# Kernel optimization log

Measured on AMD Instinct MI355X. Metric: run time of the kernel, lower is better.

Reference implementation:

```python
import jax, jax.numpy as jnp
import numpy as np


def setup_inputs() -> dict:
    key = jax.random.key(0)
    ks = jax.random.split(key, 9)
    B, C, H, W = 4, 256, 128, 128
    d = C // 8
    x = jax.random.normal(ks[0], (B, C, H, W), jnp.float32)
    wq = jax.random.normal(ks[1], (d, C), jnp.float32) * 0.05
    bq = jax.random.normal(ks[2], (d,), jnp.float32) * 0.05
    wk = jax.random.normal(ks[3], (d, C), jnp.float32) * 0.05
    bk = jax.random.normal(ks[4], (d,), jnp.float32) * 0.05
    wv = jax.random.normal(ks[5], (d, C), jnp.float32) * 0.05
    bv = jax.random.normal(ks[6], (d,), jnp.float32) * 0.05
    wp = jax.random.normal(ks[7], (C, d, 3, 3), jnp.float32) * 0.05
    gamma = jax.random.normal(ks[8], (1,), jnp.float32)
    return dict(x=x, wq=wq, bq=bq, wk=wk, bk=bk, wv=wv, bv=bv, wp=wp, gamma=gamma)


def reference(x, wq, bq, wk, bk, wv, bv, wp, gamma):
    B, C, H, W = x.shape
    d = wq.shape[0]  # C // 8
    N = H * W
    # 1x1 convs expressed as channel matmuls
    q = jnp.einsum('bchw,dc->bdhw', x, wq) + bq[None, :, None, None]
    k = jnp.einsum('bchw,dc->bdhw', x, wk) + bk[None, :, None, None]
    v = jnp.einsum('bchw,dc->bdhw', x, wv) + bv[None, :, None, None]
    Q = q.reshape(B, d, N)
    K = k.reshape(B, d, N)
    V = v.reshape(B, d, N)
    # channel-channel energy: [B, d, d]
    energy = jnp.einsum('bdn,ben->bde', Q, K)
    energy_new = jnp.max(energy, axis=-1, keepdims=True) - energy
    attention = jax.nn.softmax(energy_new, axis=-1)
    out = jnp.einsum('bde,ben->bdn', attention, V).reshape(B, d, H, W)
    # 3x3 conv (no bias) + exact GELU
    out = jax.lax.conv_general_dilated(
        out, wp, window_strides=(1, 1), padding='SAME',
        dimension_numbers=('NCHW', 'OIHW', 'NCHW'))
    out = jax.nn.gelu(out, approximate=False)
    return gamma[0] * out + x
```

## Files before the change

### kernel.cpp

```cpp
#include <hip/hip_runtime.h>
#include <hip/hip_bf16.h>
#include <math.h>

#define BB 4
#define CC 256
#define HH 128
#define WW 128
#define NN (HH*WW)
#define DD 32

#define AOT_CI   44
#define AOT_ROWE (130*AOT_CI)
#define AOT_IMGE (130*AOT_ROWE)
#define AOT_BYTES ((size_t)BB*AOT_IMGE*2)
#define AOT_ALLOC (AOT_BYTES + 1024)

#define WT_BYTES (9*256*AOT_CI*2)

#define PATCH_SZ 45760
#define WSLAB    22528
#define CONV_LDS (PATCH_SZ + 2*WSLAB)
#define EPI_PITCH 260

#define ASWZ_BYTES 98304
#define AHALF      49152
#define QK2        132

typedef __attribute__((ext_vector_type(8)))  short bf16x8;
typedef __attribute__((ext_vector_type(4)))  float f32x4;
typedef __attribute__((ext_vector_type(16))) float f32x16;

__device__ inline void async_copy16(void* lds, const void* g) {
    __builtin_amdgcn_global_load_lds(
        (const __attribute__((address_space(1))) unsigned int*)g,
        (__attribute__((address_space(3))) unsigned int*)lds, 16, 0, 0);
}

__device__ inline unsigned short f2bf(float f) {
    __hip_bfloat16 h = __float2bfloat16(f);
    return *reinterpret_cast<unsigned short*>(&h);
}

__device__ inline void split2(float v, unsigned short& h, unsigned short& l) {
    __hip_bfloat16 hb = __float2bfloat16(v);
    float r = v - __bfloat162float(hb);
    __hip_bfloat16 lb = __float2bfloat16(r);
    h = *reinterpret_cast<unsigned short*>(&hb);
    l = *reinterpret_cast<unsigned short*>(&lb);
}

__device__ inline bf16x8 ld_frag8(const char* p) {
    union { bf16x8 v; short4 h[2]; } u;
    u.h[0] = *(const short4*)(p);
    u.h[1] = *(const short4*)(p + 8);
    return u.v;
}

__device__ inline float gelu_fast(float v) {
    float a = fabsf(v) * 0.70710678118654752f;
    float t = __fdividef(1.0f, fmaf(0.3275911f, a, 1.0f));
    float p = t * fmaf(t, fmaf(t, fmaf(t, fmaf(t, 1.061405429f, -1.453152027f),
                                       1.421413741f), -0.284496736f), 0.254829592f);
    float e = 1.0f - p * __expf(-a * a);
    float erfv = (v < 0.0f) ? -e : e;
    return 0.5f * v * (1.0f + erfv);
}

__global__ __launch_bounds__(256) void prep_kernel(
    const float* __restrict__ wp, unsigned short* __restrict__ Wt,
    const float* __restrict__ wq, const float* __restrict__ wk,
    const float* __restrict__ wv, unsigned short* __restrict__ Aswz,
    unsigned short* __restrict__ AOT)
{
    const int blk = blockIdx.x;
    if (blk < 288) {
        int i = blk*256 + threadIdx.x;
        int kk = i / (256*32);
        int r  = i % (256*32);
        int co = r >> 5, ci = r & 31;
        float v = wp[((size_t)co*32 + ci)*9 + kk];
        Wt[((size_t)kk*256 + co)*AOT_CI + ci] = f2bf(v);
    } else if (blk < 480) {
        int i = (blk-288)*256 + threadIdx.x;
        int j    = i & 7;
        int lane = (i >> 3) & 63;
        int cf   = (i >> 9) % 3;
        int s    = i / 1536;
        int row  = cf*32 + (lane & 31);
        int k    = s*16 + (lane >> 5)*8 + j;
        int c    = k >> 1;
        float w  = (row < 32) ? wq[row*256 + c]
                 : (row < 64) ? wk[(row-32)*256 + c]
                              : wv[(row-64)*256 + c];
        unsigned short h, l;
        split2(w, h, l);
        Aswz[i] = (k & 1) ? l : h;
    } else {
        int idx = (blk-480)*256 + threadIdx.x;
        if (idx < BB*22704) {
            int b = idx / 22704;
            int r = idx % 22704;
            size_t off;
            if (r < 11440) {
                int row = (r < 5720) ? 0 : 129;
                int e   = (r < 5720) ? r : r - 5720;
                off = (size_t)b*AOT_IMGE + (size_t)row*AOT_ROWE + e;
            } else {
                int r2 = r - 11440;
                int rr = r2 / 88 + 1;
                int w2 = r2 % 88;
                int col = (w2 < 44) ? 0 : 129;
                int ci  = (w2 < 44) ? w2 : w2 - 44;
                off = (size_t)b*AOT_IMGE + (size_t)rr*AOT_ROWE
                    + (size_t)col*AOT_CI + ci;
            }
            AOT[off] = 0;
        }
    }
}

__global__ __launch_bounds__(256, 4) void qkv_mfma_kernel(
    const float* __restrict__ x, const unsigned short* __restrict__ Aswz,
    const float* __restrict__ bq, const float* __restrict__ bk,
    const float* __restrict__ bv,
    float* __restrict__ Vout, float* __restrict__ Ep)
{
    __shared__ __align__(16) char lds[AHALF];
    __shared__ float biasL[96];
    const int b    = blockIdx.y;
    const int s    = blockIdx.x;
    const int n0   = s * 128;
    const int tid  = threadIdx.x;
    const int lane = tid & 63;
    const int wid  = tid >> 6;
    const int l31  = lane & 31;
    const int lh   = lane >> 5;
    const int nloc = 32*wid + l31;

    for (int i = tid; i < 3072; i += 256)
        async_copy16(lds + i*16, (const char*)Aswz + i*16);
    if (tid < 96)
        biasL[tid] = (tid < 32) ? bq[tid] : (tid < 64) ? bk[tid-32] : bv[tid-64];

    const float* xlane = x + ((size_t)b*CC + 4*lh)*NN + (n0 + nloc);

    f32x16 acc0 = {0}, acc1 = {0}, acc2 = {0};

    float xq[4][4];
    #pragma unroll
    for (int p0 = 0; p0 < 4; ++p0) {
        const float* p = xlane + (size_t)(8*p0)*NN;
        xq[p0][0] = p[0];            xq[p0][1] = p[(size_t)NN];
        xq[p0][2] = p[(size_t)2*NN]; xq[p0][3] = p[(size_t)3*NN];
    }

    auto run_half = [&](int st_base) {
        for (int su = 0; su < 16; su += 4) {
            #pragma unroll
            for (int ph = 0; ph < 4; ++ph) {
                const int stl = su + ph;
                const int st  = st_base + stl;
                const char* ab = lds + (size_t)(stl*3)*1024 + lane*16;
                bf16x8 a0 = *(const bf16x8*)(ab);
                bf16x8 a1 = *(const bf16x8*)(ab + 1024);
                bf16x8 a2 = *(const bf16x8*)(ab + 2048);
                float v0 = xq[ph][0], v1 = xq[ph][1];
                float v2 = xq[ph][2], v3 = xq[ph][3];
                if (st + 4 < 32) {
                    const float* p = xlane + (size_t)(8*(st+4))*NN;
                    xq[ph][0] = p[0];            xq[ph][1] = p[(size_t)NN];
                    xq[ph][2] = p[(size_t)2*NN]; xq[ph][3] = p[(size_t)3*NN];
                }
                union { bf16x8 v; unsigned int u[4]; } B1, B2;
                #pragma unroll
                for (int j = 0; j < 4; ++j) {
                    float vj = (j==0)?v0:(j==1)?v1:(j==2)?v2:v3;
                    unsigned int hb = __float_as_uint(vj) & 0xFFFF0000u;
                    float rj = vj - __uint_as_float(hb);
                    unsigned int lb = __float_as_uint(rj) >> 16;
                    B1.u[j] = hb | (hb >> 16);
                    B2.u[j] = lb | (lb << 16);
                }
                acc0 = __builtin_amdgcn_mfma_f32_32x32x16_bf16(a0, B1.v, acc0, 0, 0, 0);
                acc1 = __builtin_amdgcn_mfma_f32_32x32x16_bf16(a1, B1.v, acc1, 0, 0, 0);
                acc2 = __builtin_amdgcn_mfma_f32_32x32x16_bf16(a2, B1.v, acc2, 0, 0, 0);
                acc0 = __builtin_amdgcn_mfma_f32_32x32x16_bf16(a0, B2.v, acc0, 0, 0, 0);
                acc1 = __builtin_amdgcn_mfma_f32_32x32x16_bf16(a1, B2.v, acc1, 0, 0, 0);
                acc2 = __builtin_amdgcn_mfma_f32_32x32x16_bf16(a2, B2.v, acc2, 0, 0, 0);
            }
        }
    };

    __syncthreads();
    run_half(0);
    __syncthreads();
    for (int i = tid; i < 3072; i += 256)
        async_copy16(lds + i*16, (const char*)Aswz + AHALF + i*16);
    __syncthreads();
    run_half(16);

    __syncthreads();
    float* qk = (float*)lds;
    #pragma unroll
    for (int r = 0; r < 16; ++r) {
        const int rsub = (r & 3) + 8*(r >> 2) + 4*lh;
        qk[rsub*QK2 + nloc]      = acc0[r] + biasL[rsub];
        qk[(32+rsub)*QK2 + nloc] = acc1[r] + biasL[32+rsub];
        Vout[((size_t)b*DD + rsub)*NN + n0 + nloc] = acc2[r] + biasL[64+rsub];
    }
    __syncthreads();

    const int d  = tid >> 3;
    const int e0 = tid & 7;
    const float* qrow = qk + d*QK2;
    float s0 = 0.f, s1 = 0.f, s2 = 0.f, s3 = 0.f;
    for (int n4 = 0; n4 < 128; n4 += 4) {
        float4 qv = *(const float4*)(qrow + n4);
        float4 k0 = *(const float4*)(qk + (32 + e0     )*QK2 + n4);
        float4 k1 = *(const float4*)(qk + (32 + e0 +  8)*QK2 + n4);
        float4 k2 = *(const float4*)(qk + (32 + e0 + 16)*QK2 + n4);
        float4 k3 = *(const float4*)(qk + (32 + e0 + 24)*QK2 + n4);
        s0 += qv.x*k0.x + qv.y*k0.y + qv.z*k0.z + qv.w*k0.w;
        s1 += qv.x*k1.x + qv.y*k1.y + qv.z*k1.z + qv.w*k1.w;
        s2 += qv.x*k2.x + qv.y*k2.y + qv.z*k2.z + qv.w*k2.w;
        s3 += qv.x*k3.x + qv.y*k3.y + qv.z*k3.z + qv.w*k3.w;
    }
    float* ep = Ep + ((size_t)s*BB + b)*1024;
    ep[d*32 + e0]      = s0;
    ep[d*32 + e0 + 8]  = s1;
    ep[d*32 + e0 + 16] = s2;
    ep[d*32 + e0 + 24] = s3;
}

__global__ __launch_bounds__(1024) void softmax_kernel(
    const float* __restrict__ Ep, float* __restrict__ attT)
{
    const int b = blockIdx.x;
    const int e = threadIdx.x, d = threadIdx.y;
    float s = 0.f;
    for (int p = 0; p < 128; ++p)
        s += Ep[((size_t)p * BB + b) * (DD * DD) + d * DD + e];
    float nv = -s;
    float m = nv;
    for (int off = 16; off > 0; off >>= 1) m = fmaxf(m, __shfl_xor(m, off, 32));
    float pe = expf(nv - m);
    float su = pe;
    for (int off = 16; off > 0; off >>= 1) su += __shfl_xor(su, off, 32);
    attT[(size_t)b * (DD * DD) + e * DD + d] = pe / su;
}

__global__ __launch_bounds__(256) void pv_kernel(
    const float* __restrict__ V, const float* __restrict__ attT,
    unsigned short* __restrict__ AOT)
{
    __shared__ float Vs[DD][128];
    __shared__ float at4[DD][DD];
    const int b  = blockIdx.y;
    const int n0 = blockIdx.x * 128;
    const int tid = threadIdx.x;
    for (int i = tid; i < 1024; i += 256) {
        int r = i >> 5, c4 = i & 31;
        *(float4*)&Vs[r][c4*4] =
            *(const float4*)(V + ((size_t)b*DD + r)*NN + n0 + c4*4);
    }
    for (int i = tid; i < 1024; i += 256)
        at4[i >> 5][i & 31] = attT[(size_t)b*1024 + i];
    __syncthreads();
    const int nl = tid & 127;
    const int dg = tid >> 7;
    float acc[16];
    #pragma unroll
    for (int k = 0; k < 16; ++k) acc[k] = 0.f;
    #pragma unroll 4
    for (int e = 0; e < DD; ++e) {
        float v = Vs[e][nl];
        const float4* ar = (const float4*)&at4[e][dg*16];
        #pragma unroll
        for (int q = 0; q < 4; ++q) {
            float4 a = ar[q];
            acc[4*q+0] += a.x * v; acc[4*q+1] += a.y * v;
            acc[4*q+2] += a.z * v; acc[4*q+3] += a.w * v;
        }
    }
    const int n = n0 + nl;
    const int h = n >> 7, w = n & 127;
    unsigned short* dst = AOT + (size_t)b*AOT_IMGE + (size_t)(h+1)*AOT_ROWE
                              + (size_t)(w+1)*AOT_CI + dg*16;
    #pragma unroll
    for (int q = 0; q < 4; ++q) {
        ushort4 u;
        u.x = f2bf(acc[4*q+0]); u.y = f2bf(acc[4*q+1]);
        u.z = f2bf(acc[4*q+2]); u.w = f2bf(acc[4*q+3]);
        *(ushort4*)(dst + 4*q) = u;
    }
}

__global__ __launch_bounds__(512, 1) void conv_kernel(
    const unsigned short* __restrict__ AOT, const unsigned short* __restrict__ Wt,
    const float* __restrict__ gammap, const float* __restrict__ x,
    float* __restrict__ out)
{
    __shared__ __align__(16) char lds[CONV_LDS];
    const int b   = blockIdx.y;
    const int h0  = blockIdx.x * 2;
    const int tid = threadIdx.x;
    const int wid = tid >> 6;
    const int lane = tid & 63;
    const int l15 = lane & 15;
    const int lj  = lane >> 4;
    const int wn  = wid & 1;
    const int wc  = wid >> 1;

    const char* psrc = (const char*)(AOT + (size_t)b*AOT_IMGE + (size_t)h0*AOT_ROWE);
    for (int i = tid; i < PATCH_SZ/16; i += 512)
        async_copy16(lds + i*16, psrc + i*16);
    for (int i = tid; i < WSLAB/16; i += 512)
        async_copy16(lds + PATCH_SZ + i*16, (const char*)Wt + i*16);
    __syncthreads();

    f32x4 acc[4][8];
    #pragma unroll
    for (int cf = 0; cf < 4; ++cf)
        #pragma unroll
        for (int nf = 0; nf < 8; ++nf)
            acc[cf][nf] = (f32x4){0.f, 0.f, 0.f, 0.f};

    for (int kk = 0; kk < 9; ++kk) {
        if (kk < 8) {
            const char* wsrc = (const char*)Wt + (size_t)(kk+1)*WSLAB;
            char* wdst = lds + PATCH_SZ + ((kk+1)&1)*WSLAB;
            for (int i = tid; i < WSLAB/16; i += 512)
                async_copy16(wdst + i*16, wsrc + i*16);
        }
        const int kh = kk / 3, kw = kk % 3;
        const char* wbase = lds + PATCH_SZ + (kk&1)*WSLAB;
        bf16x8 af[4];
        #pragma unroll
        for (int cf = 0; cf < 4; ++cf)
            af[cf] = ld_frag8(wbase + (wc*64 + cf*16 + l15)*88 + lj*16);
        #pragma unroll
        for (int nf = 0; nf < 8; ++nf) {
            const int cell = (wn + kh)*130 + nf*16 + l15 + kw;
            const bf16x8 bfr = ld_frag8(lds + cell*88 + lj*16);
            #pragma unroll
            for (int cf = 0; cf < 4; ++cf)
                acc[cf][nf] = __builtin_amdgcn_mfma_f32_16x16x32_bf16(
                    af[cf], bfr, acc[cf][nf], 0, 0, 0);
        }
        __syncthreads();
    }

    const float g0 = gammap[0];
    float* lf = (float*)lds;
    for (int k = 0; k < 4; ++k) {
        if (wc == k) {
            #pragma unroll
            for (int cf = 0; cf < 4; ++cf) {
                const int rl = cf*16 + 4*lj;
                #pragma unroll
                for (int nf = 0; nf < 8; ++nf) {
                    const int col = wn*128 + nf*16 + l15;
                    #pragma unroll
                    for (int j = 0; j < 4; ++j)
                        lf[(rl + j)*EPI_PITCH + col] = acc[cf][nf][j];
                }
            }
        }
        __syncthreads();
        #pragma unroll
        for (int it = 0; it < 8; ++it) {
            const int idx = tid + it*512;
            const int row = idx >> 6, c4 = idx & 63;
            const int co  = k*64 + row;
            const size_t g = ((size_t)b*CC + co)*NN + (size_t)h0*WW + c4*4;
            float4 v  = *(const float4*)(lf + row*EPI_PITCH + c4*4);
            float4 xv = *(const float4*)(x + g);
            float4 o;
            o.x = g0*gelu_fast(v.x) + xv.x;
            o.y = g0*gelu_fast(v.y) + xv.y;
            o.z = g0*gelu_fast(v.z) + xv.z;
            o.w = g0*gelu_fast(v.w) + xv.w;
            *(float4*)(out + g) = o;
        }
        __syncthreads();
    }
}

extern "C" void kernel_launch(void* const* d_in, const int* in_sizes, int n_in,
                              void* d_out, int out_size, void* d_ws, size_t ws_size,
                              hipStream_t stream)
{
    const float* x  = (const float*)d_in[0];
    const float* wq = (const float*)d_in[1];
    const float* bq = (const float*)d_in[2];
    const float* wk = (const float*)d_in[3];
    const float* bk = (const float*)d_in[4];
    const float* wv = (const float*)d_in[5];
    const float* bv = (const float*)d_in[6];
    const float* wp = (const float*)d_in[7];
    const float* gm = (const float*)d_in[8];
    float* out = (float*)d_out;

    float* Vbuf = out;

    char* ws = (char*)d_ws;
    unsigned short* AOT  = (unsigned short*)ws;
    unsigned short* Wt   = (unsigned short*)(ws + AOT_ALLOC);
    unsigned short* Aswz = (unsigned short*)(ws + AOT_ALLOC + WT_BYTES);
    float* Ep  = (float*)(ws + AOT_ALLOC + WT_BYTES + ASWZ_BYTES);
    float* ATT = Ep + (size_t)128*BB*1024;

    prep_kernel    <<<dim3(1024), 256, 0, stream>>>(wp, Wt, wq, wk, wv, Aswz, AOT);
    qkv_mfma_kernel<<<dim3(128, BB), 256, 0, stream>>>(x, Aswz, bq, bk, bv, Vbuf, Ep);
    softmax_kernel <<<dim3(BB), dim3(32, 32), 0, stream>>>(Ep, ATT);
    pv_kernel      <<<dim3(128, BB), 256, 0, stream>>>(Vbuf, ATT, AOT);
    conv_kernel    <<<dim3(64, BB), 512, 0, stream>>>(AOT, Wt, gm, x, out);
}
```

Measured before the change: 85.89 us.

## Split QKV projection into single-wave blocks and move energy to separate kernel

The QKV projection now runs as 2048 single-wavefront blocks of 32 columns each. These read the swizzled weights straight from global memory with register prefetch instead of staging them in LDS, and write Q, K and V to a scratch region in the output buffer. A new energy kernel computes per-slice Q·K^T partials from that buffer with 4x4 register tiles, reduced across four wavefronts in LDS, producing 64 partials instead of 128. This raises parallelism and removes LDS/barrier overhead from the projection, at the cost of an extra kernel launch and a global round trip for Q and K (about 16 MB more traffic).

```diff
diff --git a/kernel.cpp b/kernel.cpp
--- a/kernel.cpp
+++ b/kernel.cpp
@@ -23,8 +23,6 @@
 #define EPI_PITCH 260
 
 #define ASWZ_BYTES 98304
-#define AHALF      49152
-#define QK2        132
 
 typedef __attribute__((ext_vector_type(8)))  short bf16x8;
 typedef __attribute__((ext_vector_type(4)))  float f32x4;
@@ -119,117 +117,136 @@
     }
 }
 
-__global__ __launch_bounds__(256, 4) void qkv_mfma_kernel(
+__global__ __launch_bounds__(64) void qkv_mfma_kernel(
     const float* __restrict__ x, const unsigned short* __restrict__ Aswz,
     const float* __restrict__ bq, const float* __restrict__ bk,
-    const float* __restrict__ bv,
-    float* __restrict__ Vout, float* __restrict__ Ep)
-{
-    __shared__ __align__(16) char lds[AHALF];
-    __shared__ float biasL[96];
+    const float* __restrict__ bv, float* __restrict__ QKV)
+{
     const int b    = blockIdx.y;
     const int s    = blockIdx.x;
-    const int n0   = s * 128;
-    const int tid  = threadIdx.x;
-    const int lane = tid & 63;
-    const int wid  = tid >> 6;
+    const int n0   = s * 32;
+    const int lane = threadIdx.x;
     const int l31  = lane & 31;
     const int lh   = lane >> 5;
-    const int nloc = 32*wid + l31;
-
-    for (int i = tid; i < 3072; i += 256)
-        async_copy16(lds + i*16, (const char*)Aswz + i*16);
-    if (tid < 96)
-        biasL[tid] = (tid < 32) ? bq[tid] : (tid < 64) ? bk[tid-32] : bv[tid-64];
-
-    const float* xlane = x + ((size_t)b*CC + 4*lh)*NN + (n0 + nloc);
+
+    const float* xlane = x + ((size_t)b*CC + 4*lh)*NN + (n0 + l31);
+    const bf16x8* Ab = (const bf16x8*)Aswz;
 
     f32x16 acc0 = {0}, acc1 = {0}, acc2 = {0};
 
-    float xq[4][4];
-    #pragma unroll
-    for (int p0 = 0; p0 < 4; ++p0) {
+    float xq[8][4];
+    #pragma unroll
+    for (int p0 = 0; p0 < 8; ++p0) {
         const float* p = xlane + (size_t)(8*p0)*NN;
         xq[p0][0] = p[0];            xq[p0][1] = p[(size_t)NN];
         xq[p0][2] = p[(size_t)2*NN]; xq[p0][3] = p[(size_t)3*NN];
     }
-
-    auto run_half = [&](int st_base) {
-        for (int su = 0; su < 16; su += 4) {
+    bf16x8 aq[2][3];
+    #pragma unroll
+    for (int p0 = 0; p0 < 2; ++p0) {
+        aq[p0][0] = Ab[(p0*3 + 0)*64 + lane];
+        aq[p0][1] = Ab[(p0*3 + 1)*64 + lane];
+        aq[p0][2] = Ab[(p0*3 + 2)*64 + lane];
+    }
+
+    for (int g = 0; g < 4; ++g) {
+        #pragma unroll
+        for (int ph = 0; ph < 8; ++ph) {
+            const int st = g*8 + ph;
+            bf16x8 a0 = aq[ph & 1][0];
+            bf16x8 a1 = aq[ph & 1][1];
+            bf16x8 a2 = aq[ph & 1][2];
+            if (st + 2 < 32) {
+                aq[ph & 1][0] = Ab[((st+2)*3 + 0)*64 + lane];
+                aq[ph & 1][1] = Ab[((st+2)*3 + 1)*64 + lane];
+                aq[ph & 1][2] = Ab[((st+2)*3 + 2)*64 + lane];
+            }
+            float v0 = xq[ph][0], v1 = xq[ph][1];
+            float v2 = xq[ph][2], v3 = xq[ph][3];
+            if (st + 8 < 32) {
+                const float* p = xlane + (size_t)(8*(st+8))*NN;
+                xq[ph][0] = p[0];            xq[ph][1] = p[(size_t)NN];
+                xq[ph][2] = p[(size_t)2*NN]; xq[ph][3] = p[(size_t)3*NN];
+            }
+            union { bf16x8 v; unsigned int u[4]; } B1, B2;
             #pragma unroll
-            for (int ph = 0; ph < 4; ++ph) {
-                const int stl = su + ph;
-                const int st  = st_base + stl;
-                const char* ab = lds + (size_t)(stl*3)*1024 + lane*16;
-                bf16x8 a0 = *(const bf16x8*)(ab);
-                bf16x8 a1 = *(const bf16x8*)(ab + 1024);
-                bf16x8 a2 = *(const bf16x8*)(ab + 2048);
-                float v0 = xq[ph][0], v1 = xq[ph][1];
-                float v2 = xq[ph][2], v3 = xq[ph][3];
-                if (st + 4 < 32) {
-                    const float* p = xlane + (size_t)(8*(st+4))*NN;
-                    xq[ph][0] = p[0];            xq[ph][1] = p[(size_t)NN];
-                    xq[ph][2] = p[(size_t)2*NN]; xq[ph][3] = p[(size_t)3*NN];
-                }
-                union { bf16x8 v; unsigned int u[4]; } B1, B2;
-                #pragma unroll
-                for (int j = 0; j < 4; ++j) {
-                    float vj = (j==0)?v0:(j==1)?v1:(j==2)?v2:v3;
-                    unsigned int hb = __float_as_uint(vj) & 0xFFFF0000u;
-                    float rj = vj - __uint_as_float(hb);
-                    unsigned int lb = __float_as_uint(rj) >> 16;
-                    B1.u[j] = hb | (hb >> 16);
-                    B2.u[j] = lb | (lb << 16);
-                }
-                acc0 = __builtin_amdgcn_mfma_f32_32x32x16_bf16(a0, B1.v, acc0, 0, 0, 0);
-                acc1 = __builtin_amdgcn_mfma_f32_32x32x16_bf16(a1, B1.v, acc1, 0, 0, 0);
-                acc2 = __builtin_amdgcn_mfma_f32_32x32x16_bf16(a2, B1.v, acc2, 0, 0, 0);
-                acc0 = __builtin_amdgcn_mfma_f32_32x32x16_bf16(a0, B2.v, acc0, 0, 0, 0);
-                acc1 = __builtin_amdgcn_mfma_f32_32x32x16_bf16(a1, B2.v, acc1, 0, 0, 0);
-                acc2 = __builtin_amdgcn_mfma_f32_32x32x16_bf16(a2, B2.v, acc2, 0, 0, 0);
+            for (int j = 0; j < 4; ++j) {
+                float vj = (j==0)?v0:(j==1)?v1:(j==2)?v2:v3;
+                unsigned int hb = __float_as_uint(vj) & 0xFFFF0000u;
+                float rj = vj - __uint_as_float(hb);
+                unsigned int lb = __float_as_uint(rj) >> 16;
+                B1.u[j] = hb | (hb >> 16);
+                B2.u[j] = lb | (lb << 16);
             }
-        }
-    };
-
+            acc0 = __builtin_amdgcn_mfma_f32_32x32x16_bf16(a0, B1.v, acc0, 0, 0, 0);
+            acc1 = __builtin_amdgcn_mfma_f32_32x32x16_bf16(a1, B1.v, acc1, 0, 0, 0);
+            acc2 = __builtin_amdgcn_mfma_f32_32x32x16_bf16(a2, B1.v, acc2, 0, 0, 0);
+            acc0 = __builtin_amdgcn_mfma_f32_32x32x16_bf16(a0, B2.v, acc0, 0, 0, 0);
+            acc1 = __builtin_amdgcn_mfma_f32_32x32x16_bf16(a1, B2.v, acc1, 0, 0, 0);
+            acc2 = __builtin_amdgcn_mfma_f32_32x32x16_bf16(a2, B2.v, acc2, 0, 0, 0);
+        }
+    }
+
+    float4 bq4[4], bk4[4], bv4[4];
+    #pragma unroll
+    for (int q = 0; q < 4; ++q) {
+        bq4[q] = *(const float4*)(bq + 8*q + 4*lh);
+        bk4[q] = *(const float4*)(bk + 8*q + 4*lh);
+        bv4[q] = *(const float4*)(bv + 8*q + 4*lh);
+    }
+    float* Qo = QKV + (size_t)b*96*NN + n0 + l31;
+    #pragma unroll
+    for (int r = 0; r < 16; ++r) {
+        const int q = r >> 2, j = r & 3;
+        const int rsub = j + 8*q + 4*lh;
+        const float bqv = (j==0)?bq4[q].x:(j==1)?bq4[q].y:(j==2)?bq4[q].z:bq4[q].w;
+        const float bkv = (j==0)?bk4[q].x:(j==1)?bk4[q].y:(j==2)?bk4[q].z:bk4[q].w;
+        const float bvv = (j==0)?bv4[q].x:(j==1)?bv4[q].y:(j==2)?bv4[q].z:bv4[q].w;
+        Qo[(size_t)(rsub     )*NN] = acc0[r] + bqv;
+        Qo[(size_t)(rsub + 32)*NN] = acc1[r] + bkv;
+        Qo[(size_t)(rsub + 64)*NN] = acc2[r] + bvv;
+    }
+}
+
+__global__ __launch_bounds__(256) void energy_kernel(
+    const float* __restrict__ QKV, float* __restrict__ Ep)
+{
+    __shared__ float Es[4][1024];
+    const int b  = blockIdx.y;
+    const int s  = blockIdx.x;
+    const int t  = threadIdx.x;
+    const int ns = t >> 6;
+    const int tt = t & 63;
+    const int d0 = ((tt >> 3) & 7) * 4;
+    const int e0 = (tt & 7) * 4;
+    const int n1 = s*256 + ns*64;
+    const float* Qb = QKV + (size_t)b*96*NN;
+
+    float acc[4][4] = {};
+    #pragma unroll 4
+    for (int it = 0; it < 16; ++it) {
+        const int nn = n1 + it*4;
+        float4 q4[4], k4[4];
+        #pragma unroll
+        for (int i = 0; i < 4; ++i) {
+            q4[i] = *(const float4*)(Qb + (size_t)(d0 + i)*NN + nn);
+            k4[i] = *(const float4*)(Qb + (size_t)(32 + e0 + i)*NN + nn);
+        }
+        #pragma unroll
+        for (int i = 0; i < 4; ++i)
+            #pragma unroll
+            for (int j = 0; j < 4; ++j)
+                acc[i][j] += q4[i].x*k4[j].x + q4[i].y*k4[j].y
+                           + q4[i].z*k4[j].z + q4[i].w*k4[j].w;
+    }
+    #pragma unroll
+    for (int i = 0; i < 4; ++i)
+        #pragma unroll
+        for (int j = 0; j < 4; ++j)
+            Es[ns][(d0 + i)*32 + e0 + j] = acc[i][j];
     __syncthreads();
-    run_half(0);
-    __syncthreads();
-    for (int i = tid; i < 3072; i += 256)
-        async_copy16(lds + i*16, (const char*)Aswz + AHALF + i*16);
-    __syncthreads();
-    run_half(16);
-
-    __syncthreads();
-    float* qk = (float*)lds;
-    #pragma unroll
-    for (int r = 0; r < 16; ++r) {
-        const int rsub = (r & 3) + 8*(r >> 2) + 4*lh;
-        qk[rsub*QK2 + nloc]      = acc0[r] + biasL[rsub];
-        qk[(32+rsub)*QK2 + nloc] = acc1[r] + biasL[32+rsub];
-        Vout[((size_t)b*DD + rsub)*NN + n0 + nloc] = acc2[r] + biasL[64+rsub];
-    }
-    __syncthreads();
-
-    const int d  = tid >> 3;
-    const int e0 = tid & 7;
-    const float* qrow = qk + d*QK2;
-    float s0 = 0.f, s1 = 0.f, s2 = 0.f, s3 = 0.f;
-    for (int n4 = 0; n4 < 128; n4 += 4) {
-        float4 qv = *(const float4*)(qrow + n4);
-        float4 k0 = *(const float4*)(qk + (32 + e0     )*QK2 + n4);
-        float4 k1 = *(const float4*)(qk + (32 + e0 +  8)*QK2 + n4);
-        float4 k2 = *(const float4*)(qk + (32 + e0 + 16)*QK2 + n4);
-        float4 k3 = *(const float4*)(qk + (32 + e0 + 24)*QK2 + n4);
-        s0 += qv.x*k0.x + qv.y*k0.y + qv.z*k0.z + qv.w*k0.w;
-        s1 += qv.x*k1.x + qv.y*k1.y + qv.z*k1.z + qv.w*k1.w;
-        s2 += qv.x*k2.x + qv.y*k2.y + qv.z*k2.z + qv.w*k2.w;
-        s3 += qv.x*k3.x + qv.y*k3.y + qv.z*k3.z + qv.w*k3.w;
-    }
-    float* ep = Ep + ((size_t)s*BB + b)*1024;
-    ep[d*32 + e0]      = s0;
-    ep[d*32 + e0 + 8]  = s1;
-    ep[d*32 + e0 + 16] = s2;
-    ep[d*32 + e0 + 24] = s3;
+    for (int i = t; i < 1024; i += 256)
+        Ep[((size_t)s*BB + b)*1024 + i] = Es[0][i] + Es[1][i] + Es[2][i] + Es[3][i];
 }
 
 __global__ __launch_bounds__(1024) void softmax_kernel(
@@ -238,7 +255,7 @@
     const int b = blockIdx.x;
     const int e = threadIdx.x, d = threadIdx.y;
     float s = 0.f;
-    for (int p = 0; p < 128; ++p)
+    for (int p = 0; p < 64; ++p)
         s += Ep[((size_t)p * BB + b) * (DD * DD) + d * DD + e];
     float nv = -s;
     float m = nv;
@@ -250,7 +267,7 @@
 }
 
 __global__ __launch_bounds__(256) void pv_kernel(
-    const float* __restrict__ V, const float* __restrict__ attT,
+    const float* __restrict__ QKV, const float* __restrict__ attT,
     unsigned short* __restrict__ AOT)
 {
     __shared__ float Vs[DD][128];
@@ -261,7 +278,7 @@
     for (int i = tid; i < 1024; i += 256) {
         int r = i >> 5, c4 = i & 31;
         *(float4*)&Vs[r][c4*4] =
-            *(const float4*)(V + ((size_t)b*DD + r)*NN + n0 + c4*4);
+            *(const float4*)(QKV + ((size_t)b*96 + 64 + r)*NN + n0 + c4*4);
     }
     for (int i = tid; i < 1024; i += 256)
         at4[i >> 5][i & 31] = attT[(size_t)b*1024 + i];
@@ -401,18 +418,19 @@
     const float* gm = (const float*)d_in[8];
     float* out = (float*)d_out;
 
-    float* Vbuf = out;
+    float* QKV = out;
 
     char* ws = (char*)d_ws;
     unsigned short* AOT  = (unsigned short*)ws;
     unsigned short* Wt   = (unsigned short*)(ws + AOT_ALLOC);
     unsigned short* Aswz = (unsigned short*)(ws + AOT_ALLOC + WT_BYTES);
     float* Ep  = (float*)(ws + AOT_ALLOC + WT_BYTES + ASWZ_BYTES);
-    float* ATT = Ep + (size_t)128*BB*1024;
+    float* ATT = Ep + (size_t)64*BB*1024;
 
     prep_kernel    <<<dim3(1024), 256, 0, stream>>>(wp, Wt, wq, wk, wv, Aswz, AOT);
-    qkv_mfma_kernel<<<dim3(128, BB), 256, 0, stream>>>(x, Aswz, bq, bk, bv, Vbuf, Ep);
+    qkv_mfma_kernel<<<dim3(512, BB), 64, 0, stream>>>(x, Aswz, bq, bk, bv, QKV);
+    energy_kernel  <<<dim3(64, BB), 256, 0, stream>>>(QKV, Ep);
     softmax_kernel <<<dim3(BB), dim3(32, 32), 0, stream>>>(Ep, ATT);
-    pv_kernel      <<<dim3(128, BB), 256, 0, stream>>>(Vbuf, ATT, AOT);
+    pv_kernel      <<<dim3(128, BB), 256, 0, stream>>>(QKV, ATT, AOT);
     conv_kernel    <<<dim3(64, BB), 512, 0, stream>>>(AOT, Wt, gm, x, out);
 }
```

Result: slower. 88.45 us (+3.0%).

## Split QKV projection over channels across waves and add two-stage energy reduction

Applied to the files above, without the earlier changes.

The QKV MFMA kernel now handles 32 pixels per block instead of 128, with each of the four waves covering a quarter of the 256 input channels. The waves' partial accumulators are summed through LDS, and A fragments are read straight from global memory with double-buffered registers instead of being staged into LDS. This gives a grid four times larger for better CU occupancy and shorter per-wave dependency chains. The cost is 512 partial energy blocks per batch, so a new ereduce kernel folds them down to 64 before softmax, adding a launch and extra global traffic.

```diff
diff --git a/kernel.cpp b/kernel.cpp
--- a/kernel.cpp
+++ b/kernel.cpp
@@ -23,8 +23,7 @@
 #define EPI_PITCH 260
 
 #define ASWZ_BYTES 98304
-#define AHALF      49152
-#define QK2        132
+#define QKPITCH 36
 
 typedef __attribute__((ext_vector_type(8)))  short bf16x8;
 typedef __attribute__((ext_vector_type(4)))  float f32x4;
@@ -119,107 +118,119 @@
     }
 }
 
-__global__ __launch_bounds__(256, 4) void qkv_mfma_kernel(
+__global__ __launch_bounds__(256) void qkv_mfma_kernel(
     const float* __restrict__ x, const unsigned short* __restrict__ Aswz,
     const float* __restrict__ bq, const float* __restrict__ bk,
     const float* __restrict__ bv,
     float* __restrict__ Vout, float* __restrict__ Ep)
 {
-    __shared__ __align__(16) char lds[AHALF];
-    __shared__ float biasL[96];
+    __shared__ __align__(16) float lds_f[4*3072 + 96];
     const int b    = blockIdx.y;
     const int s    = blockIdx.x;
-    const int n0   = s * 128;
+    const int n0   = s * 32;
     const int tid  = threadIdx.x;
+    const int w    = tid >> 6;
     const int lane = tid & 63;
-    const int wid  = tid >> 6;
     const int l31  = lane & 31;
     const int lh   = lane >> 5;
-    const int nloc = 32*wid + l31;
-
-    for (int i = tid; i < 3072; i += 256)
-        async_copy16(lds + i*16, (const char*)Aswz + i*16);
+
+    float* biasL = lds_f + 12288;
     if (tid < 96)
         biasL[tid] = (tid < 32) ? bq[tid] : (tid < 64) ? bk[tid-32] : bv[tid-64];
 
-    const float* xlane = x + ((size_t)b*CC + 4*lh)*NN + (n0 + nloc);
+    const float* xlane = x + ((size_t)b*CC + 64*w + 4*lh)*NN + (n0 + l31);
+    const bf16x8* Ab = (const bf16x8*)Aswz;
+    const int st0 = 8*w;
+
+    float xq[8][4];
+    #pragma unroll
+    for (int p = 0; p < 8; ++p) {
+        const float* pp = xlane + (size_t)(8*p)*NN;
+        xq[p][0] = pp[0];            xq[p][1] = pp[(size_t)NN];
+        xq[p][2] = pp[(size_t)2*NN]; xq[p][3] = pp[(size_t)3*NN];
+    }
+    bf16x8 aq[2][3];
+    #pragma unroll
+    for (int p = 0; p < 2; ++p) {
+        aq[p][0] = Ab[((st0+p)*3 + 0)*64 + lane];
+        aq[p][1] = Ab[((st0+p)*3 + 1)*64 + lane];
+        aq[p][2] = Ab[((st0+p)*3 + 2)*64 + lane];
+    }
 
     f32x16 acc0 = {0}, acc1 = {0}, acc2 = {0};
-
-    float xq[4][4];
-    #pragma unroll
-    for (int p0 = 0; p0 < 4; ++p0) {
-        const float* p = xlane + (size_t)(8*p0)*NN;
-        xq[p0][0] = p[0];            xq[p0][1] = p[(size_t)NN];
-        xq[p0][2] = p[(size_t)2*NN]; xq[p0][3] = p[(size_t)3*NN];
-    }
-
-    auto run_half = [&](int st_base) {
-        for (int su = 0; su < 16; su += 4) {
-            #pragma unroll
-            for (int ph = 0; ph < 4; ++ph) {
-                const int stl = su + ph;
-                const int st  = st_base + stl;
-                const char* ab = lds + (size_t)(stl*3)*1024 + lane*16;
-                bf16x8 a0 = *(const bf16x8*)(ab);
-                bf16x8 a1 = *(const bf16x8*)(ab + 1024);
-                bf16x8 a2 = *(const bf16x8*)(ab + 2048);
-                float v0 = xq[ph][0], v1 = xq[ph][1];
-                float v2 = xq[ph][2], v3 = xq[ph][3];
-                if (st + 4 < 32) {
-                    const float* p = xlane + (size_t)(8*(st+4))*NN;
-                    xq[ph][0] = p[0];            xq[ph][1] = p[(size_t)NN];
-                    xq[ph][2] = p[(size_t)2*NN]; xq[ph][3] = p[(size_t)3*NN];
-                }
-                union { bf16x8 v; unsigned int u[4]; } B1, B2;
-                #pragma unroll
-                for (int j = 0; j < 4; ++j) {
-                    float vj = (j==0)?v0:(j==1)?v1:(j==2)?v2:v3;
-                    unsigned int hb = __float_as_uint(vj) & 0xFFFF0000u;
-                    float rj = vj - __uint_as_float(hb);
-                    unsigned int lb = __float_as_uint(rj) >> 16;
-                    B1.u[j] = hb | (hb >> 16);
-                    B2.u[j] = lb | (lb << 16);
-                }
-                acc0 = __builtin_amdgcn_mfma_f32_32x32x16_bf16(a0, B1.v, acc0, 0, 0, 0);
-                acc1 = __builtin_amdgcn_mfma_f32_32x32x16_bf16(a1, B1.v, acc1, 0, 0, 0);
-                acc2 = __builtin_amdgcn_mfma_f32_32x32x16_bf16(a2, B1.v, acc2, 0, 0, 0);
-                acc0 = __builtin_amdgcn_mfma_f32_32x32x16_bf16(a0, B2.v, acc0, 0, 0, 0);
-                acc1 = __builtin_amdgcn_mfma_f32_32x32x16_bf16(a1, B2.v, acc1, 0, 0, 0);
-                acc2 = __builtin_amdgcn_mfma_f32_32x32x16_bf16(a2, B2.v, acc2, 0, 0, 0);
-            }
-        }
-    };
-
+    #pragma unroll
+    for (int ph = 0; ph < 8; ++ph) {
+        bf16x8 a0 = aq[ph & 1][0];
+        bf16x8 a1 = aq[ph & 1][1];
+        bf16x8 a2 = aq[ph & 1][2];
+        if (ph < 6) {
+            aq[ph & 1][0] = Ab[((st0+ph+2)*3 + 0)*64 + lane];
+            aq[ph & 1][1] = Ab[((st0+ph+2)*3 + 1)*64 + lane];
+            aq[ph & 1][2] = Ab[((st0+ph+2)*3 + 2)*64 + lane];
+        }
+        union { bf16x8 v; unsigned int u[4]; } B1, B2;
+        #pragma unroll
+        for (int j = 0; j < 4; ++j) {
+            float vj = xq[ph][j];
+            unsigned int hb = __float_as_uint(vj) & 0xFFFF0000u;
+            float rj = vj - __uint_as_float(hb);
+            unsigned int lb = __float_as_uint(rj) >> 16;
+            B1.u[j] = hb | (hb >> 16);
+            B2.u[j] = lb | (lb << 16);
+        }
+        acc0 = __builtin_amdgcn_mfma_f32_32x32x16_bf16(a0, B1.v, acc0, 0, 0, 0);
+        acc1 = __builtin_amdgcn_mfma_f32_32x32x16_bf16(a1, B1.v, acc1, 0, 0, 0);
+        acc2 = __builtin_amdgcn_mfma_f32_32x32x16_bf16(a2, B1.v, acc2, 0, 0, 0);
+        acc0 = __builtin_amdgcn_mfma_f32_32x32x16_bf16(a0, B2.v, acc0, 0, 0, 0);
+        acc1 = __builtin_amdgcn_mfma_f32_32x32x16_bf16(a1, B2.v, acc1, 0, 0, 0);
+        acc2 = __builtin_amdgcn_mfma_f32_32x32x16_bf16(a2, B2.v, acc2, 0, 0, 0);
+    }
+
+    float* slab = lds_f + w*3072;
+    #pragma unroll
+    for (int r = 0; r < 16; ++r) {
+        slab[(     r)*64 + lane] = acc0[r];
+        slab[(16 + r)*64 + lane] = acc1[r];
+        slab[(32 + r)*64 + lane] = acc2[r];
+    }
     __syncthreads();
-    run_half(0);
+
+    float sums[12];
+    #pragma unroll
+    for (int i = 0; i < 12; ++i) {
+        const int idx = tid + i*256;
+        const int row = idx >> 5, n = idx & 31;
+        const int cf = row >> 5, rsub = row & 31;
+        const int r   = ((rsub >> 3) << 2) | (rsub & 3);
+        const int lh2 = (rsub >> 2) & 1;
+        const int fo  = (cf*16 + r)*64 + lh2*32 + n;
+        sums[i] = lds_f[fo] + lds_f[3072 + fo] + lds_f[6144 + fo]
+                + lds_f[9216 + fo] + biasL[row];
+    }
     __syncthreads();
-    for (int i = tid; i < 3072; i += 256)
-        async_copy16(lds + i*16, (const char*)Aswz + AHALF + i*16);
-    __syncthreads();
-    run_half(16);
-
-    __syncthreads();
-    float* qk = (float*)lds;
-    #pragma unroll
-    for (int r = 0; r < 16; ++r) {
-        const int rsub = (r & 3) + 8*(r >> 2) + 4*lh;
-        qk[rsub*QK2 + nloc]      = acc0[r] + biasL[rsub];
-        qk[(32+rsub)*QK2 + nloc] = acc1[r] + biasL[32+rsub];
-        Vout[((size_t)b*DD + rsub)*NN + n0 + nloc] = acc2[r] + biasL[64+rsub];
+
+    #pragma unroll
+    for (int i = 0; i < 12; ++i) {
+        const int idx = tid + i*256;
+        const int row = idx >> 5, n = idx & 31;
+        if (row < 64)
+            lds_f[row*QKPITCH + n] = sums[i];
+        else
+            Vout[((size_t)b*DD + (row-64))*NN + n0 + n] = sums[i];
     }
     __syncthreads();
 
     const int d  = tid >> 3;
     const int e0 = tid & 7;
-    const float* qrow = qk + d*QK2;
+    const float* qrow = lds_f + d*QKPITCH;
     float s0 = 0.f, s1 = 0.f, s2 = 0.f, s3 = 0.f;
-    for (int n4 = 0; n4 < 128; n4 += 4) {
+    #pragma unroll
+    for (int n4 = 0; n4 < 32; n4 += 4) {
         float4 qv = *(const float4*)(qrow + n4);
-        float4 k0 = *(const float4*)(qk + (32 + e0     )*QK2 + n4);
-        float4 k1 = *(const float4*)(qk + (32 + e0 +  8)*QK2 + n4);
-        float4 k2 = *(const float4*)(qk + (32 + e0 + 16)*QK2 + n4);
-        float4 k3 = *(const float4*)(qk + (32 + e0 + 24)*QK2 + n4);
+        float4 k0 = *(const float4*)(lds_f + (32 + e0     )*QKPITCH + n4);
+        float4 k1 = *(const float4*)(lds_f + (32 + e0 +  8)*QKPITCH + n4);
+        float4 k2 = *(const float4*)(lds_f + (32 + e0 + 16)*QKPITCH + n4);
+        float4 k3 = *(const float4*)(lds_f + (32 + e0 + 24)*QKPITCH + n4);
         s0 += qv.x*k0.x + qv.y*k0.y + qv.z*k0.z + qv.w*k0.w;
         s1 += qv.x*k1.x + qv.y*k1.y + qv.z*k1.z + qv.w*k1.w;
         s2 += qv.x*k2.x + qv.y*k2.y + qv.z*k2.z + qv.w*k2.w;
@@ -232,13 +243,27 @@
     ep[d*32 + e0 + 24] = s3;
 }
 
+__global__ __launch_bounds__(256) void ereduce_kernel(
+    const float* __restrict__ Ep, float* __restrict__ Epr)
+{
+    const int b = blockIdx.y, S = blockIdx.x;
+    const int t = threadIdx.x;
+    float4 a = {0.f, 0.f, 0.f, 0.f};
+    #pragma unroll
+    for (int p = 0; p < 8; ++p) {
+        float4 v = *(const float4*)(Ep + ((size_t)(S*8 + p)*BB + b)*1024 + t*4);
+        a.x += v.x; a.y += v.y; a.z += v.z; a.w += v.w;
+    }
+    *(float4*)(Epr + ((size_t)S*BB + b)*1024 + t*4) = a;
+}
+
 __global__ __launch_bounds__(1024) void softmax_kernel(
     const float* __restrict__ Ep, float* __restrict__ attT)
 {
     const int b = blockIdx.x;
     const int e = threadIdx.x, d = threadIdx.y;
     float s = 0.f;
-    for (int p = 0; p < 128; ++p)
+    for (int p = 0; p < 64; ++p)
         s += Ep[((size_t)p * BB + b) * (DD * DD) + d * DD + e];
     float nv = -s;
     float m = nv;
@@ -408,11 +433,13 @@
     unsigned short* Wt   = (unsigned short*)(ws + AOT_ALLOC);
     unsigned short* Aswz = (unsigned short*)(ws + AOT_ALLOC + WT_BYTES);
     float* Ep  = (float*)(ws + AOT_ALLOC + WT_BYTES + ASWZ_BYTES);
-    float* ATT = Ep + (size_t)128*BB*1024;
+    float* Epr = Ep + (size_t)512*BB*1024;
+    float* ATT = Epr + (size_t)64*BB*1024;
 
     prep_kernel    <<<dim3(1024), 256, 0, stream>>>(wp, Wt, wq, wk, wv, Aswz, AOT);
-    qkv_mfma_kernel<<<dim3(128, BB), 256, 0, stream>>>(x, Aswz, bq, bk, bv, Vbuf, Ep);
-    softmax_kernel <<<dim3(BB), dim3(32, 32), 0, stream>>>(Ep, ATT);
+    qkv_mfma_kernel<<<dim3(512, BB), 256, 0, stream>>>(x, Aswz, bq, bk, bv, Vbuf, Ep);
+    ereduce_kernel <<<dim3(64, BB), 256, 0, stream>>>(Ep, Epr);
+    softmax_kernel <<<dim3(BB), dim3(32, 32), 0, stream>>>(Epr, ATT);
     pv_kernel      <<<dim3(128, BB), 256, 0, stream>>>(Vbuf, ATT, AOT);
     conv_kernel    <<<dim3(64, BB), 512, 0, stream>>>(AOT, Wt, gm, x, out);
 }
```

Measured after the change: 83.37 us. -2.9%, faster.

## Restructure QKV kernel with coalesced float4 x loads staged through LDS

Applied to the files above, without the earlier changes.

The QKV projection kernel now uses 512-thread blocks covering 256 pixels each. Each block loads the full hi/lo-split weight matrix into LDS once instead of in two halves. Activations are read as coalesced float4 vectors, split into bf16 hi/lo pairs and written to a double-buffered LDS staging area with a three-deep register prefetch, rather than scalar strided loads per lane. The weight layout in prep is rearranged to match, and the number of partial energy tiles drops to 64, which also halves the softmax reduction loop. The cost is a large LDS footprint giving one block per CU, plus a barrier on every channel step.

```diff
diff --git a/kernel.cpp b/kernel.cpp
--- a/kernel.cpp
+++ b/kernel.cpp
@@ -23,8 +23,8 @@
 #define EPI_PITCH 260
 
 #define ASWZ_BYTES 98304
-#define AHALF      49152
-#define QK2        132
+#define QKVP 260
+#define QKV_LDS 131584
 
 typedef __attribute__((ext_vector_type(8)))  short bf16x8;
 typedef __attribute__((ext_vector_type(4)))  float f32x4;
@@ -47,6 +47,14 @@
     __hip_bfloat16 lb = __float2bfloat16(r);
     h = *reinterpret_cast<unsigned short*>(&hb);
     l = *reinterpret_cast<unsigned short*>(&lb);
+}
+
+__device__ inline unsigned int packsplit(float v) {
+    unsigned int fb = __float_as_uint(v);
+    unsigned int hb = fb & 0xFFFF0000u;
+    float r = v - __uint_as_float(hb);
+    unsigned int lb = __float_as_uint(r) >> 16;
+    return (hb >> 16) | (lb << 16);
 }
 
 __device__ inline bf16x8 ld_frag8(const char* p) {
@@ -84,17 +92,19 @@
         int i = (blk-288)*256 + threadIdx.x;
         int j    = i & 7;
         int lane = (i >> 3) & 63;
-        int cf   = (i >> 9) % 3;
-        int s    = i / 1536;
+        int q9   = i >> 9;
+        int cf   = q9 % 3;
+        int t    = q9 / 3;
+        int hl   = t & 1;
+        int s    = t >> 1;
         int row  = cf*32 + (lane & 31);
-        int k    = s*16 + (lane >> 5)*8 + j;
-        int c    = k >> 1;
+        int c    = s*16 + (lane >> 5)*8 + j;
         float w  = (row < 32) ? wq[row*256 + c]
                  : (row < 64) ? wk[(row-32)*256 + c]
                               : wv[(row-64)*256 + c];
         unsigned short h, l;
         split2(w, h, l);
-        Aswz[i] = (k & 1) ? l : h;
+        Aswz[i] = hl ? l : h;
     } else {
         int idx = (blk-480)*256 + threadIdx.x;
         if (idx < BB*22704) {
@@ -119,117 +129,120 @@
     }
 }
 
-__global__ __launch_bounds__(256, 4) void qkv_mfma_kernel(
+__global__ __launch_bounds__(512, 1) void qkv_mfma_kernel(
     const float* __restrict__ x, const unsigned short* __restrict__ Aswz,
     const float* __restrict__ bq, const float* __restrict__ bk,
     const float* __restrict__ bv,
     float* __restrict__ Vout, float* __restrict__ Ep)
 {
-    __shared__ __align__(16) char lds[AHALF];
-    __shared__ float biasL[96];
+    __shared__ __align__(16) char lds[QKV_LDS];
     const int b    = blockIdx.y;
     const int s    = blockIdx.x;
-    const int n0   = s * 128;
+    const int n0   = s * 256;
     const int tid  = threadIdx.x;
+    const int w    = tid >> 6;
     const int lane = tid & 63;
-    const int wid  = tid >> 6;
     const int l31  = lane & 31;
     const int lh   = lane >> 5;
-    const int nloc = 32*wid + l31;
-
-    for (int i = tid; i < 3072; i += 256)
+    const int ch_a = tid >> 6;
+    const int f4   = tid & 63;
+
+    for (int i = tid; i < 6144; i += 512)
         async_copy16(lds + i*16, (const char*)Aswz + i*16);
+    float* biasL = (float*)(lds + 131072);
     if (tid < 96)
         biasL[tid] = (tid < 32) ? bq[tid] : (tid < 64) ? bk[tid-32] : bv[tid-64];
 
-    const float* xlane = x + ((size_t)b*CC + 4*lh)*NN + (n0 + nloc);
+    unsigned int* stg[2] = { (unsigned int*)(lds + 98304),
+                             (unsigned int*)(lds + 114688) };
+    const float* xb = x + (size_t)b*CC*NN + n0 + f4*4;
 
     f32x16 acc0 = {0}, acc1 = {0}, acc2 = {0};
 
-    float xq[4][4];
+    float4 va0, vb0, va1, vb1, va2, vb2;
+    #define LOADX(VA, VB, R) do { \
+        VA = *(const float4*)(xb + (size_t)((R)*16 + ch_a    )*NN); \
+        VB = *(const float4*)(xb + (size_t)((R)*16 + ch_a + 8)*NN); } while (0)
+    #define PACKW(BUF, VA, VB) do { \
+        uint4 ua, ub; \
+        ua.x = packsplit((VA).x); ua.y = packsplit((VA).y); \
+        ua.z = packsplit((VA).z); ua.w = packsplit((VA).w); \
+        ub.x = packsplit((VB).x); ub.y = packsplit((VB).y); \
+        ub.z = packsplit((VB).z); ub.w = packsplit((VB).w); \
+        *(uint4*)((BUF) + (ch_a    )*256 + f4*4) = ua; \
+        *(uint4*)((BUF) + (ch_a + 8)*256 + f4*4) = ub; } while (0)
+
+    LOADX(va0, vb0, 0);
+    LOADX(va1, vb1, 1);
+    LOADX(va2, vb2, 2);
+    PACKW(stg[0], va0, vb0);
+    __syncthreads();
+
     #pragma unroll
-    for (int p0 = 0; p0 < 4; ++p0) {
-        const float* p = xlane + (size_t)(8*p0)*NN;
-        xq[p0][0] = p[0];            xq[p0][1] = p[(size_t)NN];
-        xq[p0][2] = p[(size_t)2*NN]; xq[p0][3] = p[(size_t)3*NN];
-    }
-
-    auto run_half = [&](int st_base) {
-        for (int su = 0; su < 16; su += 4) {
+    for (int r = 0; r < 16; ++r) {
+        {
+            const unsigned int* bufc = stg[r & 1];
+            unsigned int u[8];
             #pragma unroll
-            for (int ph = 0; ph < 4; ++ph) {
-                const int stl = su + ph;
-                const int st  = st_base + stl;
-                const char* ab = lds + (size_t)(stl*3)*1024 + lane*16;
-                bf16x8 a0 = *(const bf16x8*)(ab);
-                bf16x8 a1 = *(const bf16x8*)(ab + 1024);
-                bf16x8 a2 = *(const bf16x8*)(ab + 2048);
-                float v0 = xq[ph][0], v1 = xq[ph][1];
-                float v2 = xq[ph][2], v3 = xq[ph][3];
-                if (st + 4 < 32) {
-                    const float* p = xlane + (size_t)(8*(st+4))*NN;
-                    xq[ph][0] = p[0];            xq[ph][1] = p[(size_t)NN];
-                    xq[ph][2] = p[(size_t)2*NN]; xq[ph][3] = p[(size_t)3*NN];
-                }
-                union { bf16x8 v; unsigned int u[4]; } B1, B2;
-                #pragma unroll
-                for (int j = 0; j < 4; ++j) {
-                    float vj = (j==0)?v0:(j==1)?v1:(j==2)?v2:v3;
-                    unsigned int hb = __float_as_uint(vj) & 0xFFFF0000u;
-                    float rj = vj - __uint_as_float(hb);
-                    unsigned int lb = __float_as_uint(rj) >> 16;
-                    B1.u[j] = hb | (hb >> 16);
-                    B2.u[j] = lb | (lb << 16);
-                }
-                acc0 = __builtin_amdgcn_mfma_f32_32x32x16_bf16(a0, B1.v, acc0, 0, 0, 0);
-                acc1 = __builtin_amdgcn_mfma_f32_32x32x16_bf16(a1, B1.v, acc1, 0, 0, 0);
-                acc2 = __builtin_amdgcn_mfma_f32_32x32x16_bf16(a2, B1.v, acc2, 0, 0, 0);
-                acc0 = __builtin_amdgcn_mfma_f32_32x32x16_bf16(a0, B2.v, acc0, 0, 0, 0);
-                acc1 = __builtin_amdgcn_mfma_f32_32x32x16_bf16(a1, B2.v, acc1, 0, 0, 0);
-                acc2 = __builtin_amdgcn_mfma_f32_32x32x16_bf16(a2, B2.v, acc2, 0, 0, 0);
+            for (int j = 0; j < 8; ++j)
+                u[j] = bufc[(lh*8 + j)*256 + 32*w + l31];
+            union { bf16x8 v; unsigned int d[4]; } B1, B2;
+            #pragma unroll
+            for (int dq = 0; dq < 4; ++dq) {
+                B1.d[dq] = (u[2*dq] & 0xFFFFu)      | (u[2*dq+1] << 16);
+                B2.d[dq] = (u[2*dq] >> 16)          | (u[2*dq+1] & 0xFFFF0000u);
             }
-        }
-    };
-
-    __syncthreads();
-    run_half(0);
-    __syncthreads();
-    for (int i = tid; i < 3072; i += 256)
-        async_copy16(lds + i*16, (const char*)Aswz + AHALF + i*16);
-    __syncthreads();
-    run_half(16);
-
-    __syncthreads();
+            #pragma unroll
+            for (int cf = 0; cf < 3; ++cf) {
+                bf16x8 ah = *(const bf16x8*)(lds + (((r*6 +     cf)*64) + lane)*16);
+                bf16x8 al = *(const bf16x8*)(lds + (((r*6 + 3 + cf)*64) + lane)*16);
+                f32x16* ac = (cf == 0) ? &acc0 : (cf == 1) ? &acc1 : &acc2;
+                *ac = __builtin_amdgcn_mfma_f32_32x32x16_bf16(ah, B1.v, *ac, 0, 0, 0);
+                *ac = __builtin_amdgcn_mfma_f32_32x32x16_bf16(ah, B2.v, *ac, 0, 0, 0);
+                *ac = __builtin_amdgcn_mfma_f32_32x32x16_bf16(al, B1.v, *ac, 0, 0, 0);
+                *ac = __builtin_amdgcn_mfma_f32_32x32x16_bf16(al, B2.v, *ac, 0, 0, 0);
+            }
+        }
+        if (r < 15) {
+            if ((r+1) % 3 == 0)      PACKW(stg[(r+1) & 1], va0, vb0);
+            else if ((r+1) % 3 == 1) PACKW(stg[(r+1) & 1], va1, vb1);
+            else                     PACKW(stg[(r+1) & 1], va2, vb2);
+        }
+        if (r + 3 < 16) {
+            if ((r+3) % 3 == 0)      LOADX(va0, vb0, r+3);
+            else if ((r+3) % 3 == 1) LOADX(va1, vb1, r+3);
+            else                     LOADX(va2, vb2, r+3);
+        }
+        __syncthreads();
+    }
+
     float* qk = (float*)lds;
     #pragma unroll
     for (int r = 0; r < 16; ++r) {
         const int rsub = (r & 3) + 8*(r >> 2) + 4*lh;
-        qk[rsub*QK2 + nloc]      = acc0[r] + biasL[rsub];
-        qk[(32+rsub)*QK2 + nloc] = acc1[r] + biasL[32+rsub];
-        Vout[((size_t)b*DD + rsub)*NN + n0 + nloc] = acc2[r] + biasL[64+rsub];
+        const int col  = 32*w + l31;
+        qk[rsub*QKVP + col]      = acc0[r] + biasL[rsub];
+        qk[(32+rsub)*QKVP + col] = acc1[r] + biasL[32 + rsub];
+        Vout[((size_t)b*DD + rsub)*NN + n0 + col] = acc2[r] + biasL[64 + rsub];
     }
     __syncthreads();
 
-    const int d  = tid >> 3;
-    const int e0 = tid & 7;
-    const float* qrow = qk + d*QK2;
-    float s0 = 0.f, s1 = 0.f, s2 = 0.f, s3 = 0.f;
-    for (int n4 = 0; n4 < 128; n4 += 4) {
+    const int d  = tid >> 4;
+    const int e2 = tid & 15;
+    const float* qrow = qk + d*QKVP;
+    float s0 = 0.f, s1 = 0.f;
+    for (int n4 = 0; n4 < 256; n4 += 4) {
         float4 qv = *(const float4*)(qrow + n4);
-        float4 k0 = *(const float4*)(qk + (32 + e0     )*QK2 + n4);
-        float4 k1 = *(const float4*)(qk + (32 + e0 +  8)*QK2 + n4);
-        float4 k2 = *(const float4*)(qk + (32 + e0 + 16)*QK2 + n4);
-        float4 k3 = *(const float4*)(qk + (32 + e0 + 24)*QK2 + n4);
-        s0 += qv.x*k0.x + qv.y*k0.y + qv.z*k0.z + qv.w*k0.w;
-        s1 += qv.x*k1.x + qv.y*k1.y + qv.z*k1.z + qv.w*k1.w;
-        s2 += qv.x*k2.x + qv.y*k2.y + qv.z*k2.z + qv.w*k2.w;
-        s3 += qv.x*k3.x + qv.y*k3.y + qv.z*k3.z + qv.w*k3.w;
+        float4 ka = *(const float4*)(qk + (32 + e2)*QKVP + n4);
+        float4 kb = *(const float4*)(qk + (48 + e2)*QKVP + n4);
+        s0 += qv.x*ka.x + qv.y*ka.y + qv.z*ka.z + qv.w*ka.w;
+        s1 += qv.x*kb.x + qv.y*kb.y + qv.z*kb.z + qv.w*kb.w;
     }
     float* ep = Ep + ((size_t)s*BB + b)*1024;
-    ep[d*32 + e0]      = s0;
-    ep[d*32 + e0 + 8]  = s1;
-    ep[d*32 + e0 + 16] = s2;
-    ep[d*32 + e0 + 24] = s3;
+    ep[d*32 + e2]      = s0;
+    ep[d*32 + e2 + 16] = s1;
+    #undef LOADX
+    #undef PACKW
 }
 
 __global__ __launch_bounds__(1024) void softmax_kernel(
@@ -238,7 +251,8 @@
     const int b = blockIdx.x;
     const int e = threadIdx.x, d = threadIdx.y;
     float s = 0.f;
-    for (int p = 0; p < 128; ++p)
+    #pragma unroll 8
+    for (int p = 0; p < 64; ++p)
         s += Ep[((size_t)p * BB + b) * (DD * DD) + d * DD + e];
     float nv = -s;
     float m = nv;
@@ -283,9 +297,9 @@
         }
     }
     const int n = n0 + nl;
-    const int h = n >> 7, w = n & 127;
+    const int h = n >> 7, ww = n & 127;
     unsigned short* dst = AOT + (size_t)b*AOT_IMGE + (size_t)(h+1)*AOT_ROWE
-                              + (size_t)(w+1)*AOT_CI + dg*16;
+                              + (size_t)(ww+1)*AOT_CI + dg*16;
     #pragma unroll
     for (int q = 0; q < 4; ++q) {
         ushort4 u;
@@ -408,10 +422,10 @@
     unsigned short* Wt   = (unsigned short*)(ws + AOT_ALLOC);
     unsigned short* Aswz = (unsigned short*)(ws + AOT_ALLOC + WT_BYTES);
     float* Ep  = (float*)(ws + AOT_ALLOC + WT_BYTES + ASWZ_BYTES);
-    float* ATT = Ep + (size_t)128*BB*1024;
+    float* ATT = Ep + (size_t)64*BB*1024;
 
     prep_kernel    <<<dim3(1024), 256, 0, stream>>>(wp, Wt, wq, wk, wv, Aswz, AOT);
-    qkv_mfma_kernel<<<dim3(128, BB), 256, 0, stream>>>(x, Aswz, bq, bk, bv, Vbuf, Ep);
+    qkv_mfma_kernel<<<dim3(64, BB), 512, 0, stream>>>(x, Aswz, bq, bk, bv, Vbuf, Ep);
     softmax_kernel <<<dim3(BB), dim3(32, 32), 0, stream>>>(Ep, ATT);
     pv_kernel      <<<dim3(128, BB), 256, 0, stream>>>(Vbuf, ATT, AOT);
     conv_kernel    <<<dim3(64, BB), 512, 0, stream>>>(AOT, Wt, gm, x, out);
```

New measurement: 79.89 us. 1.08x faster.
